# Performance work log

Hardware: AMD Instinct MI355X
Metric: run time of the kernel (lower is better)

## Reference

```python
import jax, jax.numpy as jnp
import numpy as np
from jax import lax

C = 256      # in_c == out_c == dim
NH = 8       # num_heads
K = 7        # depthwise pos-enc kernel
H1 = 512     # int(mlp_ratio * in_c) = 2.0 * 256
B, Hs, Ws = 2, 48, 48


def setup_inputs() -> dict:
    key = jax.random.key(0)
    ks = jax.random.split(key, 8)
    w = lambda k, shape: jax.random.normal(k, shape, jnp.float32) * 0.02
    return {
        "x": jax.random.normal(ks[0], (B, C, Hs, Ws), jnp.float32),
        # 1x1 convs stored as [out, in] (BN folded into weight+bias)
        "qk_w": w(ks[1], (2 * C, C)), "qk_b": jnp.zeros((2 * C,), jnp.float32),
        "v_w": w(ks[2], (C, C)),       "v_b": jnp.zeros((C,), jnp.float32),
        # depthwise positional encoding conv [C,1,K,K]
        "pe_w": w(ks[3], (C, 1, K, K)), "pe_b": jnp.zeros((C,), jnp.float32),
        "proj_w": w(ks[4], (C, C)),    "proj_b": jnp.zeros((C,), jnp.float32),
        # conv FFN: 1x1 (SiLU) -> 1x1 (no act)
        "fc1_w": w(ks[5], (H1, C)),    "fc1_b": jnp.zeros((H1,), jnp.float32),
        "fc2_w": w(ks[6], (C, H1)),    "fc2_b": jnp.zeros((C,), jnp.float32),
    }


def _c1(x, w, b):
    # 1x1 conv == per-pixel matmul
    return jnp.einsum('bchw,oc->bohw', x, w) + b[None, :, None, None]


def reference(x, qk_w, qk_b, v_w, v_b, pe_w, pe_b, proj_w, proj_b,
              fc1_w, fc1_b, fc2_w, fc2_b):
    Bb, Cc, Hh, Ww = x.shape
    hd = Cc // NH                 # head_dim = 32
    N = Hh * Ww
    scale = hd ** -0.5

    # ---- AttentionV2 ----
    qk = _c1(x, qk_w, qk_b).reshape(Bb, NH, 2 * hd, N)
    q, k = qk[:, :, :hd], qk[:, :, hd:]
    v_full = _c1(x, v_w, v_b)                      # [B,C,H,W]
    pe = lax.conv_general_dilated(
        v_full, pe_w, (1, 1), 'SAME', feature_group_count=Cc,
        dimension_numbers=('NCHW', 'OIHW', 'NCHW')) + pe_b[None, :, None, None]
    v = v_full.reshape(Bb, NH, hd, N)

    # attn = q^T @ k * scale ; softmax over keys
    attn = jax.nn.softmax(jnp.einsum('bhdn,bhdm->bhnm', q, k) * scale, axis=-1)
    o = jnp.einsum('bhdm,bhnm->bhdn', v, attn).reshape(Bb, Cc, Hh, Ww)
    attn_out = _c1(o + pe, proj_w, proj_b)

    # ---- block residuals + conv FFN (add=True) ----
    x1 = x + attn_out
    h = jax.nn.silu(_c1(x1, fc1_w, fc1_b))         # Conv(in_c, hidden, 1, 1) with SiLU
    return x1 + _c1(h, fc2_w, fc2_b)               # Conv(hidden, out_c, 1, act=False)
```

## Files before the change

kernel.cpp:

```cpp
#include <hip/hip_runtime.h>
#include <hip/hip_bf16.h>

#define NCH 256
#define NHD 8
#define HD 32
#define NPIX 2304
#define H1DIM 512

typedef __attribute__((ext_vector_type(8))) __bf16 bf16x8;
typedef __attribute__((ext_vector_type(4))) float f32x4;

__global__ __launch_bounds__(256) void prep_k(
    const float* __restrict__ x,
    const float* __restrict__ w0, const float* __restrict__ w1,
    const float* __restrict__ w2, const float* __restrict__ w3,
    const float* __restrict__ w4,
    __bf16* __restrict__ Xb, __bf16* __restrict__ Wall) {
    const int tid = threadIdx.x;
    if (blockIdx.x < 288) {
        const int t = blockIdx.x;
        const int b = t / 144, r0 = t % 144;
        const int c0 = (r0 / 36) * 64, n0 = (r0 % 36) * 64;
        __shared__ float tile[64][65];
        const size_t sb = ((size_t)b * NCH + c0) * NPIX + n0;
#pragma unroll
        for (int i = 0; i < 16; ++i) {
            int idx = tid + i * 256;
            int rr = idx >> 6, cc = idx & 63;
            tile[rr][cc] = x[sb + (size_t)rr * NPIX + cc];
        }
        __syncthreads();
#pragma unroll
        for (int i = 0; i < 8; ++i) {
            int idx = tid + i * 256;
            int nn = idx >> 5, cp = (idx & 31) * 2;
            union { __bf16 h[2]; unsigned u; } pk;
            pk.h[0] = (__bf16)tile[cp][nn];
            pk.h[1] = (__bf16)tile[cp + 1][nn];
            *(unsigned*)&Xb[((size_t)b * NPIX + n0 + nn) * NCH + c0 + cp] = pk.u;
        }
    } else {
        int i = (blockIdx.x - 288) * 256 + tid;
        const float* src; int off;
        if (i < 32768)      { src = w0; off = i; }
        else if (i < 49152) { src = w1; off = i - 32768; }
        else if (i < 65536) { src = w2; off = i - 49152; }
        else if (i < 98304) { src = w3; off = i - 65536; }
        else                { src = w4; off = i - 98304; }
        float4 v = ((const float4*)src)[off];
        union { __bf16 h[4]; uint2 u; } pk;
        pk.h[0] = (__bf16)v.x; pk.h[1] = (__bf16)v.y;
        pk.h[2] = (__bf16)v.z; pk.h[3] = (__bf16)v.w;
        ((uint2*)Wall)[i] = pk.u;
    }
}

__global__ __launch_bounds__(256) void qkv_k(
    const __bf16* __restrict__ A, const __bf16* __restrict__ Wq,
    const __bf16* __restrict__ Wv, const float* __restrict__ qk_b,
    const float* __restrict__ v_b, __bf16* __restrict__ Qb,
    __bf16* __restrict__ Kf, float* __restrict__ v_bu,
    __bf16* __restrict__ Vf) {
    const int tid = threadIdx.x;
    const int wave = tid >> 6, lane = tid & 63;
    const int l16 = lane & 15, quad = lane >> 4;
    const int h = blockIdx.x & 7;
    const int u = blockIdx.x >> 3;
    const int tau = u * 4 + wave;
    const int px = tau % 144;
    const int rest = tau / 144;
    const int b = rest & 1;
    const int sub = rest >> 1;
    const int m0 = px * 16;
    const bool isv = sub >= 4;
    const int oc0 = isv ? (32 * h + 16 * (sub - 4)) : (64 * h + 16 * sub);
    const __bf16* W = isv ? Wv : Wq;

    const __bf16* aptr = A + ((size_t)b * NPIX + m0 + l16) * NCH + quad * 8;
    const __bf16* bptr = W + (size_t)(oc0 + l16) * NCH + quad * 8;

    f32x4 acc = {0.f, 0.f, 0.f, 0.f};
#pragma unroll 8
    for (int k = 0; k < NCH; k += 32) {
        bf16x8 af = *(const bf16x8*)(aptr + k);
        bf16x8 bf = *(const bf16x8*)(bptr + k);
        acc = __builtin_amdgcn_mfma_f32_16x16x32_bf16(af, bf, acc, 0, 0, 0);
    }

    const int oc = oc0 + l16;
    const int mb = m0 + quad * 4;

    if (!isv) {
        const float bb = qk_b[oc];
        const int bh = b * NHD + h;
        const int dd = (oc0 & 16) + l16;
        if ((oc0 & 32) == 0) {
            const float qs = 0.17677669529663689f * 1.4426950408889634f;
#pragma unroll
            for (int r = 0; r < 4; ++r)
                Qb[((size_t)bh * NPIX + mb + r) * 32 + dd] = (__bf16)((acc[r] + bb) * qs);
        } else {
            __bf16* kp = Kf + ((size_t)(bh * 144 + px) * 64 + (dd >> 3) * 16 + quad * 4) * 8 + (dd & 7);
#pragma unroll
            for (int r = 0; r < 4; ++r) kp[r * 8] = (__bf16)(acc[r] + bb);
        }
    } else {
        const float bb = v_b[oc];
        const int bh = b * NHD + h;
        const int half = (oc0 >> 4) & 1;
        const size_t fb = ((size_t)b * NCH + oc) * NPIX + mb;
        float4 vf_; float* vp = &vf_.x;
        union { __bf16 hh[4]; uint2 u; } pk;
#pragma unroll
        for (int r = 0; r < 4; ++r) {
            float v = acc[r] + bb;
            vp[r] = v; pk.hh[r] = (__bf16)v;
        }
        *(float4*)&v_bu[fb] = vf_;
        *(uint2*)&Vf[((size_t)(bh * 144 + px) * 64 + lane) * 8 + half * 4] = pk.u;
    }
}

__global__ __launch_bounds__(256) void dwconv_k(const float* __restrict__ vb,
                                                const float* __restrict__ pw,
                                                const float* __restrict__ pb,
                                                float* __restrict__ pe) {
    const int tid = threadIdx.x;
    const int r = (int)blockIdx.x >> 3;
    const int c = (blockIdx.x & 7) * 32 + (r & 31);
    const int b = r >> 5;
    __shared__ float plane[NPIX];
    __shared__ float wk[49];
    const size_t base = ((size_t)b * NCH + c) * NPIX;
    for (int i = tid; i < NPIX; i += 256) plane[i] = vb[base + i];
    if (tid < 49) wk[tid] = pw[c * 49 + tid];
    float bb = pb[c];
    __syncthreads();
    for (int p = tid; p < NPIX; p += 256) {
        int y = p / 48, x = p - y * 48;
        float s = bb;
#pragma unroll
        for (int ky = 0; ky < 7; ++ky) {
            int yy = y + ky - 3;
            if ((unsigned)yy < 48u) {
#pragma unroll
                for (int kx = 0; kx < 7; ++kx) {
                    int xx = x + kx - 3;
                    if ((unsigned)xx < 48u) s += wk[ky * 7 + kx] * plane[yy * 48 + xx];
                }
            }
        }
        pe[base + p] = s;
    }
}

__global__ __launch_bounds__(512) void attn6_k(const __bf16* __restrict__ Qb,
                                               const __bf16* __restrict__ Kf,
                                               const __bf16* __restrict__ Vf,
                                               const float* __restrict__ pe,
                                               __bf16* __restrict__ opb) {
    const int tid = threadIdx.x;
    const int wave = tid >> 6, lane = tid & 63;
    const int l16 = lane & 15, quad = lane >> 4;
    const int h = blockIdx.x & 7;
    const int r0 = (int)blockIdx.x >> 3;
    const int qt = r0 % 72;
    const int b = r0 / 72;
    const int qb = qt * 32;
    const int bh = b * NHD + h;

    __shared__ float o_s[8][32][33];
    __shared__ float l_s[8][32];

    bf16x8 b_q0 = *(const bf16x8*)(Qb + ((size_t)bh * NPIX + qb + l16) * 32 + quad * 8);
    bf16x8 b_q1 = *(const bf16x8*)(Qb + ((size_t)bh * NPIX + qb + 16 + l16) * 32 + quad * 8);

    const __bf16* kf = Kf + ((size_t)(bh * 144 + wave * 18) * 64 + lane) * 8;
    const __bf16* vf = Vf + ((size_t)(bh * 144 + wave * 18) * 64 + lane) * 8;

    f32x4 o00 = {0.f,0.f,0.f,0.f}, o01 = {0.f,0.f,0.f,0.f};
    f32x4 o10 = {0.f,0.f,0.f,0.f}, o11 = {0.f,0.f,0.f,0.f};
    f32x4 l0 = {0.f,0.f,0.f,0.f}, l1 = {0.f,0.f,0.f,0.f};

#pragma unroll 3
    for (int t = 0; t < 18; ++t) {
        bf16x8 a_k = *(const bf16x8*)(kf + (size_t)t * 512);
        bf16x8 va  = *(const bf16x8*)(vf + (size_t)t * 512);
        f32x4 z = {0.f, 0.f, 0.f, 0.f};
        f32x4 s0 = __builtin_amdgcn_mfma_f32_16x16x32_bf16(a_k, b_q0, z, 0, 0, 0);
        f32x4 s1 = __builtin_amdgcn_mfma_f32_16x16x32_bf16(a_k, b_q1, z, 0, 0, 0);
        f32x4 p0, p1;
#pragma unroll
        for (int r = 0; r < 4; ++r) {
            p0[r] = __builtin_amdgcn_exp2f(s0[r]);
            p1[r] = __builtin_amdgcn_exp2f(s1[r]);
        }
        l0 += p0; l1 += p1;
        bf16x8 b0lo = {}, b0hi = {}, b1lo = {}, b1hi = {};
#pragma unroll
        for (int r = 0; r < 4; ++r) {
            __bf16 c0 = (__bf16)p0[r], c1 = (__bf16)p1[r];
            b0lo[r] = c0; b0hi[4 + r] = c0;
            b1lo[r] = c1; b1hi[4 + r] = c1;
        }
        o00 = __builtin_amdgcn_mfma_f32_16x16x32_bf16(va, b0lo, o00, 0, 0, 0);
        o01 = __builtin_amdgcn_mfma_f32_16x16x32_bf16(va, b0hi, o01, 0, 0, 0);
        o10 = __builtin_amdgcn_mfma_f32_16x16x32_bf16(va, b1lo, o10, 0, 0, 0);
        o11 = __builtin_amdgcn_mfma_f32_16x16x32_bf16(va, b1hi, o11, 0, 0, 0);
    }

    float ls0 = l0[0] + l0[1] + l0[2] + l0[3];
    ls0 += __shfl_xor(ls0, 16); ls0 += __shfl_xor(ls0, 32);
    float ls1 = l1[0] + l1[1] + l1[2] + l1[3];
    ls1 += __shfl_xor(ls1, 16); ls1 += __shfl_xor(ls1, 32);

#pragma unroll
    for (int r = 0; r < 4; ++r) {
        o_s[wave][quad * 4 + r][l16]           = o00[r];
        o_s[wave][16 + quad * 4 + r][l16]      = o01[r];
        o_s[wave][quad * 4 + r][16 + l16]      = o10[r];
        o_s[wave][16 + quad * 4 + r][16 + l16] = o11[r];
    }
    if (quad == 0) { l_s[wave][l16] = ls0; l_s[wave][16 + l16] = ls1; }
    __syncthreads();

    const int q = tid & 31;
    const int d0 = (tid >> 5) * 2;
    float l = 0.f;
#pragma unroll
    for (int w = 0; w < 8; ++w) l += l_s[w][q];
    const float inv = 1.f / l;
    float v0 = 0.f, v1 = 0.f;
#pragma unroll
    for (int w = 0; w < 8; ++w) {
        v0 += o_s[w][d0][q];
        v1 += o_s[w][d0 + 1][q];
    }
    const int n = qb + q;
    const int ch = h * HD + d0;
    v0 = v0 * inv + pe[((size_t)b * NCH + ch) * NPIX + n];
    v1 = v1 * inv + pe[((size_t)b * NCH + ch + 1) * NPIX + n];
    union { __bf16 hh[2]; unsigned u; } pk;
    pk.hh[0] = (__bf16)v0; pk.hh[1] = (__bf16)v1;
    *(unsigned*)&opb[((size_t)b * NPIX + n) * NCH + ch] = pk.u;
}

__global__ __launch_bounds__(512, 2) void mlp_k(
    const __bf16* __restrict__ opb, const __bf16* __restrict__ Wp,
    const __bf16* __restrict__ W1, const __bf16* __restrict__ W2,
    const float* __restrict__ pj_b, const float* __restrict__ f1_b,
    const float* __restrict__ f2_b, const float* __restrict__ x,
    float* __restrict__ out) {
    const int tid = threadIdx.x;
    const int wave = tid >> 6, lane = tid & 63;
    const int l16 = lane & 15, quad = lane >> 4;
    const int b = (int)blockIdx.x / 144;
    const int m0 = ((int)blockIdx.x % 144) * 16;

    __shared__ __bf16 x1h[16][264];
    __shared__ __bf16 hh[16][520];

    const int oc_a = wave * 16 + l16;
    const int oc_b = oc_a + 128;
    const int row = quad * 4;
    const int mq = m0 + quad * 4;

    const __bf16* aptr = opb + ((size_t)b * NPIX + m0 + l16) * NCH + quad * 8;
    const __bf16* wp0 = Wp + (size_t)oc_a * NCH + quad * 8;
    const __bf16* wp1 = Wp + (size_t)oc_b * NCH + quad * 8;
    f32x4 a0 = {0.f, 0.f, 0.f, 0.f}, a1 = {0.f, 0.f, 0.f, 0.f};
#pragma unroll
    for (int k = 0; k < NCH; k += 32) {
        bf16x8 af = *(const bf16x8*)(aptr + k);
        a0 = __builtin_amdgcn_mfma_f32_16x16x32_bf16(af, *(const bf16x8*)(wp0 + k), a0, 0, 0, 0);
        a1 = __builtin_amdgcn_mfma_f32_16x16x32_bf16(af, *(const bf16x8*)(wp1 + k), a1, 0, 0, 0);
    }
    float x1r0[4], x1r1[4];
    {
        const float bb0 = pj_b[oc_a], bb1 = pj_b[oc_b];
        float4 xr0 = *(const float4*)&x[((size_t)b * NCH + oc_a) * NPIX + mq];
        float4 xr1 = *(const float4*)&x[((size_t)b * NCH + oc_b) * NPIX + mq];
        const float* xp0 = &xr0.x;
        const float* xp1 = &xr1.x;
#pragma unroll
        for (int r = 0; r < 4; ++r) {
            float v0 = a0[r] + bb0 + xp0[r];
            float v1 = a1[r] + bb1 + xp1[r];
            x1r0[r] = v0; x1r1[r] = v1;
            x1h[row + r][oc_a] = (__bf16)v0;
            x1h[row + r][oc_b] = (__bf16)v1;
        }
    }
    __syncthreads();

    {
        const __bf16* w10 = W1 + (size_t)oc_a * NCH + quad * 8;
        const __bf16* w11 = W1 + (size_t)(oc_a + 128) * NCH + quad * 8;
        const __bf16* w12 = W1 + (size_t)(oc_a + 256) * NCH + quad * 8;
        const __bf16* w13 = W1 + (size_t)(oc_a + 384) * NCH + quad * 8;
        f32x4 c0 = {0.f, 0.f, 0.f, 0.f}, c1 = {0.f, 0.f, 0.f, 0.f};
        f32x4 c2 = {0.f, 0.f, 0.f, 0.f}, c3 = {0.f, 0.f, 0.f, 0.f};
#pragma unroll
        for (int k = 0; k < NCH; k += 32) {
            bf16x8 af = *(const bf16x8*)&x1h[l16][quad * 8 + k];
            c0 = __builtin_amdgcn_mfma_f32_16x16x32_bf16(af, *(const bf16x8*)(w10 + k), c0, 0, 0, 0);
            c1 = __builtin_amdgcn_mfma_f32_16x16x32_bf16(af, *(const bf16x8*)(w11 + k), c1, 0, 0, 0);
            c2 = __builtin_amdgcn_mfma_f32_16x16x32_bf16(af, *(const bf16x8*)(w12 + k), c2, 0, 0, 0);
            c3 = __builtin_amdgcn_mfma_f32_16x16x32_bf16(af, *(const bf16x8*)(w13 + k), c3, 0, 0, 0);
        }
        const float g0 = f1_b[oc_a], g1 = f1_b[oc_a + 128];
        const float g2 = f1_b[oc_a + 256], g3 = f1_b[oc_a + 384];
#pragma unroll
        for (int r = 0; r < 4; ++r) {
            float v0 = c0[r] + g0; v0 = v0 / (1.f + __expf(-v0));
            float v1 = c1[r] + g1; v1 = v1 / (1.f + __expf(-v1));
            float v2 = c2[r] + g2; v2 = v2 / (1.f + __expf(-v2));
            float v3 = c3[r] + g3; v3 = v3 / (1.f + __expf(-v3));
            hh[row + r][oc_a]       = (__bf16)v0;
            hh[row + r][oc_a + 128] = (__bf16)v1;
            hh[row + r][oc_a + 256] = (__bf16)v2;
            hh[row + r][oc_a + 384] = (__bf16)v3;
        }
    }
    __syncthreads();

    {
        const __bf16* w20 = W2 + (size_t)oc_a * H1DIM + quad * 8;
        const __bf16* w21 = W2 + (size_t)oc_b * H1DIM + quad * 8;
        f32x4 d0 = {0.f, 0.f, 0.f, 0.f}, d1 = {0.f, 0.f, 0.f, 0.f};
#pragma unroll
        for (int k = 0; k < H1DIM; k += 32) {
            bf16x8 af = *(const bf16x8*)&hh[l16][quad * 8 + k];
            d0 = __builtin_amdgcn_mfma_f32_16x16x32_bf16(af, *(const bf16x8*)(w20 + k), d0, 0, 0, 0);
            d1 = __builtin_amdgcn_mfma_f32_16x16x32_bf16(af, *(const bf16x8*)(w21 + k), d1, 0, 0, 0);
        }
        const float g0 = f2_b[oc_a], g1 = f2_b[oc_b];
        float4 o0, o1;
        float* p0 = &o0.x; float* p1 = &o1.x;
#pragma unroll
        for (int r = 0; r < 4; ++r) {
            p0[r] = d0[r] + g0 + x1r0[r];
            p1[r] = d1[r] + g1 + x1r1[r];
        }
        *(float4*)&out[((size_t)b * NCH + oc_a) * NPIX + mq] = o0;
        *(float4*)&out[((size_t)b * NCH + oc_b) * NPIX + mq] = o1;
    }
}

extern "C" void kernel_launch(void* const* d_in, const int* in_sizes, int n_in,
                              void* d_out, int out_size, void* d_ws, size_t ws_size,
                              hipStream_t stream) {
    const float* x    = (const float*)d_in[0];
    const float* qk_w = (const float*)d_in[1];
    const float* qk_b = (const float*)d_in[2];
    const float* v_w  = (const float*)d_in[3];
    const float* v_b  = (const float*)d_in[4];
    const float* pe_w = (const float*)d_in[5];
    const float* pe_b = (const float*)d_in[6];
    const float* pj_w = (const float*)d_in[7];
    const float* pj_b = (const float*)d_in[8];
    const float* f1_w = (const float*)d_in[9];
    const float* f1_b = (const float*)d_in[10];
    const float* f2_w = (const float*)d_in[11];
    const float* f2_b = (const float*)d_in[12];
    float* out = (float*)d_out;

    const int B = 2;
    const size_t plane = (size_t)NCH * NPIX;
    const size_t bp = (size_t)B * plane;

    float* v_bu  = (float*)d_ws;
    float* pe_bu = v_bu + bp;
    __bf16* Xb   = (__bf16*)(pe_bu + bp);
    __bf16* opb  = Xb + bp;
    __bf16* Qb   = opb + bp;
    __bf16* Kf   = Qb + bp;
    __bf16* Vf   = Kf + bp;
    __bf16* Wall = Vf + bp;
    __bf16* Wq = Wall;
    __bf16* Wv = Wall + 131072;
    __bf16* Wp = Wall + 196608;
    __bf16* W1 = Wall + 262144;
    __bf16* W2 = Wall + 393216;

    prep_k<<<800, 256, 0, stream>>>(x, qk_w, v_w, pj_w, f1_w, f2_w, Xb, Wall);
    qkv_k<<<3456, 256, 0, stream>>>(Xb, Wq, Wv, qk_b, v_b, Qb, Kf, v_bu, Vf);
    dwconv_k<<<512, 256, 0, stream>>>(v_bu, pe_w, pe_b, pe_bu);
    attn6_k<<<1152, 512, 0, stream>>>(Qb, Kf, Vf, pe_bu, opb);
    mlp_k<<<288, 512, 0, stream>>>(opb, Wp, W1, W2, pj_b, f1_b, f2_b, x, out);
}
```

Before: 198.2 us.

## Double mlp_k block to 1024 threads and prefetch weight fragments into registers

The fused projection+FFN kernel now runs 16 waves per block, each owning half as many output channels, so per-wave MFMA chains shrink. All weight fragments for each GEMM stage are loaded into register arrays before the MFMA loop so the global loads can be in flight together. This trades higher register pressure and a stricter launch bound (1024 threads, 4 blocks) for more latency hiding in a kernel launched with only 288 blocks.

```diff
diff --git a/kernel.cpp b/kernel.cpp
--- a/kernel.cpp
+++ b/kernel.cpp
@@ -245,7 +245,7 @@
     *(unsigned*)&opb[((size_t)b * NPIX + n) * NCH + ch] = pk.u;
 }
 
-__global__ __launch_bounds__(512, 2) void mlp_k(
+__global__ __launch_bounds__(1024, 4) void mlp_k(
     const __bf16* __restrict__ opb, const __bf16* __restrict__ Wp,
     const __bf16* __restrict__ W1, const __bf16* __restrict__ W2,
     const float* __restrict__ pj_b, const float* __restrict__ f1_b,
@@ -261,89 +261,85 @@
     __shared__ __bf16 hh[16][520];
 
     const int oc_a = wave * 16 + l16;
-    const int oc_b = oc_a + 128;
     const int row = quad * 4;
     const int mq = m0 + quad * 4;
 
-    const __bf16* aptr = opb + ((size_t)b * NPIX + m0 + l16) * NCH + quad * 8;
-    const __bf16* wp0 = Wp + (size_t)oc_a * NCH + quad * 8;
-    const __bf16* wp1 = Wp + (size_t)oc_b * NCH + quad * 8;
-    f32x4 a0 = {0.f, 0.f, 0.f, 0.f}, a1 = {0.f, 0.f, 0.f, 0.f};
-#pragma unroll
-    for (int k = 0; k < NCH; k += 32) {
-        bf16x8 af = *(const bf16x8*)(aptr + k);
-        a0 = __builtin_amdgcn_mfma_f32_16x16x32_bf16(af, *(const bf16x8*)(wp0 + k), a0, 0, 0, 0);
-        a1 = __builtin_amdgcn_mfma_f32_16x16x32_bf16(af, *(const bf16x8*)(wp1 + k), a1, 0, 0, 0);
-    }
-    float x1r0[4], x1r1[4];
+    float x1r[4];
     {
-        const float bb0 = pj_b[oc_a], bb1 = pj_b[oc_b];
-        float4 xr0 = *(const float4*)&x[((size_t)b * NCH + oc_a) * NPIX + mq];
-        float4 xr1 = *(const float4*)&x[((size_t)b * NCH + oc_b) * NPIX + mq];
-        const float* xp0 = &xr0.x;
-        const float* xp1 = &xr1.x;
-#pragma unroll
-        for (int r = 0; r < 4; ++r) {
-            float v0 = a0[r] + bb0 + xp0[r];
-            float v1 = a1[r] + bb1 + xp1[r];
-            x1r0[r] = v0; x1r1[r] = v1;
-            x1h[row + r][oc_a] = (__bf16)v0;
-            x1h[row + r][oc_b] = (__bf16)v1;
+        const __bf16* aptr = opb + ((size_t)b * NPIX + m0 + l16) * NCH + quad * 8;
+        const __bf16* wp = Wp + (size_t)oc_a * NCH + quad * 8;
+        bf16x8 afr[8], wfr[8];
+#pragma unroll
+        for (int i = 0; i < 8; ++i) {
+            afr[i] = *(const bf16x8*)(aptr + i * 32);
+            wfr[i] = *(const bf16x8*)(wp + i * 32);
+        }
+        f32x4 a0 = {0.f, 0.f, 0.f, 0.f};
+#pragma unroll
+        for (int i = 0; i < 8; ++i)
+            a0 = __builtin_amdgcn_mfma_f32_16x16x32_bf16(afr[i], wfr[i], a0, 0, 0, 0);
+        const float bb = pj_b[oc_a];
+        float4 xr = *(const float4*)&x[((size_t)b * NCH + oc_a) * NPIX + mq];
+        const float* xp = &xr.x;
+#pragma unroll
+        for (int r = 0; r < 4; ++r) {
+            float v = a0[r] + bb + xp[r];
+            x1r[r] = v;
+            x1h[row + r][oc_a] = (__bf16)v;
         }
     }
     __syncthreads();
 
     {
-        const __bf16* w10 = W1 + (size_t)oc_a * NCH + quad * 8;
-        const __bf16* w11 = W1 + (size_t)(oc_a + 128) * NCH + quad * 8;
-        const __bf16* w12 = W1 + (size_t)(oc_a + 256) * NCH + quad * 8;
-        const __bf16* w13 = W1 + (size_t)(oc_a + 384) * NCH + quad * 8;
+        const __bf16* w1a = W1 + (size_t)oc_a * NCH + quad * 8;
+        const __bf16* w1b = W1 + (size_t)(oc_a + 256) * NCH + quad * 8;
+        bf16x8 wa[8], wb[8];
+#pragma unroll
+        for (int i = 0; i < 8; ++i) {
+            wa[i] = *(const bf16x8*)(w1a + i * 32);
+            wb[i] = *(const bf16x8*)(w1b + i * 32);
+        }
         f32x4 c0 = {0.f, 0.f, 0.f, 0.f}, c1 = {0.f, 0.f, 0.f, 0.f};
-        f32x4 c2 = {0.f, 0.f, 0.f, 0.f}, c3 = {0.f, 0.f, 0.f, 0.f};
-#pragma unroll
-        for (int k = 0; k < NCH; k += 32) {
-            bf16x8 af = *(const bf16x8*)&x1h[l16][quad * 8 + k];
-            c0 = __builtin_amdgcn_mfma_f32_16x16x32_bf16(af, *(const bf16x8*)(w10 + k), c0, 0, 0, 0);
-            c1 = __builtin_amdgcn_mfma_f32_16x16x32_bf16(af, *(const bf16x8*)(w11 + k), c1, 0, 0, 0);
-            c2 = __builtin_amdgcn_mfma_f32_16x16x32_bf16(af, *(const bf16x8*)(w12 + k), c2, 0, 0, 0);
-            c3 = __builtin_amdgcn_mfma_f32_16x16x32_bf16(af, *(const bf16x8*)(w13 + k), c3, 0, 0, 0);
-        }
-        const float g0 = f1_b[oc_a], g1 = f1_b[oc_a + 128];
-        const float g2 = f1_b[oc_a + 256], g3 = f1_b[oc_a + 384];
+#pragma unroll
+        for (int i = 0; i < 8; ++i) {
+            bf16x8 xf = *(const bf16x8*)&x1h[l16][quad * 8 + i * 32];
+            c0 = __builtin_amdgcn_mfma_f32_16x16x32_bf16(xf, wa[i], c0, 0, 0, 0);
+            c1 = __builtin_amdgcn_mfma_f32_16x16x32_bf16(xf, wb[i], c1, 0, 0, 0);
+        }
+        const float g0 = f1_b[oc_a], g1 = f1_b[oc_a + 256];
 #pragma unroll
         for (int r = 0; r < 4; ++r) {
             float v0 = c0[r] + g0; v0 = v0 / (1.f + __expf(-v0));
             float v1 = c1[r] + g1; v1 = v1 / (1.f + __expf(-v1));
-            float v2 = c2[r] + g2; v2 = v2 / (1.f + __expf(-v2));
-            float v3 = c3[r] + g3; v3 = v3 / (1.f + __expf(-v3));
             hh[row + r][oc_a]       = (__bf16)v0;
-            hh[row + r][oc_a + 128] = (__bf16)v1;
-            hh[row + r][oc_a + 256] = (__bf16)v2;
-            hh[row + r][oc_a + 384] = (__bf16)v3;
+            hh[row + r][oc_a + 256] = (__bf16)v1;
         }
     }
     __syncthreads();
 
     {
-        const __bf16* w20 = W2 + (size_t)oc_a * H1DIM + quad * 8;
-        const __bf16* w21 = W2 + (size_t)oc_b * H1DIM + quad * 8;
-        f32x4 d0 = {0.f, 0.f, 0.f, 0.f}, d1 = {0.f, 0.f, 0.f, 0.f};
-#pragma unroll
-        for (int k = 0; k < H1DIM; k += 32) {
-            bf16x8 af = *(const bf16x8*)&hh[l16][quad * 8 + k];
-            d0 = __builtin_amdgcn_mfma_f32_16x16x32_bf16(af, *(const bf16x8*)(w20 + k), d0, 0, 0, 0);
-            d1 = __builtin_amdgcn_mfma_f32_16x16x32_bf16(af, *(const bf16x8*)(w21 + k), d1, 0, 0, 0);
-        }
-        const float g0 = f2_b[oc_a], g1 = f2_b[oc_b];
-        float4 o0, o1;
-        float* p0 = &o0.x; float* p1 = &o1.x;
-#pragma unroll
-        for (int r = 0; r < 4; ++r) {
-            p0[r] = d0[r] + g0 + x1r0[r];
-            p1[r] = d1[r] + g1 + x1r1[r];
-        }
+        const __bf16* w2 = W2 + (size_t)oc_a * H1DIM + quad * 8;
+        f32x4 d0 = {0.f, 0.f, 0.f, 0.f};
+        bf16x8 wf[8];
+#pragma unroll
+        for (int i = 0; i < 8; ++i) wf[i] = *(const bf16x8*)(w2 + i * 32);
+#pragma unroll
+        for (int i = 0; i < 8; ++i) {
+            bf16x8 hf = *(const bf16x8*)&hh[l16][quad * 8 + i * 32];
+            d0 = __builtin_amdgcn_mfma_f32_16x16x32_bf16(hf, wf[i], d0, 0, 0, 0);
+        }
+#pragma unroll
+        for (int i = 0; i < 8; ++i) wf[i] = *(const bf16x8*)(w2 + 256 + i * 32);
+#pragma unroll
+        for (int i = 0; i < 8; ++i) {
+            bf16x8 hf = *(const bf16x8*)&hh[l16][quad * 8 + 256 + i * 32];
+            d0 = __builtin_amdgcn_mfma_f32_16x16x32_bf16(hf, wf[i], d0, 0, 0, 0);
+        }
+        const float g0 = f2_b[oc_a];
+        float4 o0; float* p0 = &o0.x;
+#pragma unroll
+        for (int r = 0; r < 4; ++r) p0[r] = d0[r] + g0 + x1r[r];
         *(float4*)&out[((size_t)b * NCH + oc_a) * NPIX + mq] = o0;
-        *(float4*)&out[((size_t)b * NCH + oc_b) * NPIX + mq] = o1;
     }
 }
 
@@ -387,5 +383,5 @@
     qkv_k<<<3456, 256, 0, stream>>>(Xb, Wq, Wv, qk_b, v_b, Qb, Kf, v_bu, Vf);
     dwconv_k<<<512, 256, 0, stream>>>(v_bu, pe_w, pe_b, pe_bu);
     attn6_k<<<1152, 512, 0, stream>>>(Qb, Kf, Vf, pe_bu, opb);
-    mlp_k<<<288, 512, 0, stream>>>(opb, Wp, W1, W2, pj_b, f1_b, f2_b, x, out);
-}
+    mlp_k<<<288, 1024, 0, stream>>>(opb, Wp, W1, W2, pj_b, f1_b, f2_b, x, out);
+}
```

Result: no change. 200.6 us (+1.2%).
